# Performance work log

Hardware: AMD Instinct MI355X
Metric: run time of the kernel (lower is better)

The kernel has to match this reference:

```python
import jax, jax.numpy as jnp
import numpy as np

N_NODES = 100000
N_EDGES = 1600000
D_IN = 128
D_EMB = 128


def setup_inputs() -> dict:
    key = jax.random.key(0)
    ks = jax.random.split(key, 8)
    x = jax.random.normal(ks[0], (N_NODES, D_IN), dtype=jnp.float32)
    src = jax.random.randint(ks[1], (N_EDGES,), 0, N_NODES, dtype=jnp.int32)
    dst = jax.random.randint(ks[2], (N_EDGES,), 0, N_NODES, dtype=jnp.int32)
    # Glorot-ish init for GraphConv weights
    s = 1.0 / np.sqrt(D_EMB)
    W0 = jax.random.normal(ks[3], (D_IN, D_EMB), dtype=jnp.float32) * s
    W1 = jax.random.normal(ks[4], (D_EMB, D_EMB), dtype=jnp.float32) * s
    W2 = jax.random.normal(ks[5], (D_EMB, D_EMB), dtype=jnp.float32) * s
    b0 = jnp.zeros((D_EMB,), jnp.float32)
    b1 = jnp.zeros((D_EMB,), jnp.float32)
    b2 = jnp.zeros((D_EMB,), jnp.float32)
    return {"x": x, "src": src, "dst": dst,
            "W0": W0, "b0": b0, "W1": W1, "b1": b1, "W2": W2, "b2": b2}


def _graph_conv(h, src, dst, norm_src, norm_dst, W, b):
    # DGL GraphConv, norm='both': D_out^{-1/2} A D_in^{-1/2} H W + b
    h = h * norm_src[:, None]                       # scale src features
    m = jax.ops.segment_sum(h[src], dst, num_segments=N_NODES)  # SpMM aggregate
    m = m * norm_dst[:, None]
    return m @ W + b


def reference(x, src, dst, W0, b0, W1, b1, W2, b2):
    ones = jnp.ones((N_EDGES,), jnp.float32)
    out_deg = jax.ops.segment_sum(ones, src, num_segments=N_NODES)
    in_deg = jax.ops.segment_sum(ones, dst, num_segments=N_NODES)
    norm_src = jax.lax.rsqrt(jnp.clip(out_deg, 1.0))
    norm_dst = jax.lax.rsqrt(jnp.clip(in_deg, 1.0))

    h = x
    Ws = (W0, W1, W2)
    bs = (b0, b1, b2)
    n_layers = len(Ws)
    for layer in range(n_layers):
        h = _graph_conv(h, src, dst, norm_src, norm_dst, Ws[layer], bs[layer])
        if layer != n_layers - 1:
            h = jax.nn.relu(h)  # dropout is identity in eval mode
    return h
```

## Files before the change

kernel.cpp:

```cpp
#include <hip/hip_runtime.h>
#include <hip/hip_bf16.h>

#define N_NODES 100000
#define N_EDGES 1600000
#define D 128
#define NB 1563
#define PB 512
#define CHUNK 3125
#define SCANL (NB * PB)
#define SGRID (SCANL / 512)
#define SENT N_NODES
#define ECAP_PAD (N_EDGES + 256 * NB)
#define BCAP 2816

typedef __attribute__((ext_vector_type(8))) short bf16x8;
typedef __attribute__((ext_vector_type(4))) float f32x4;

__device__ __forceinline__ float bf2f(unsigned short u) {
    unsigned int x = ((unsigned int)u) << 16;
    return __builtin_bit_cast(float, x);
}
__device__ __forceinline__ unsigned short f2bf(float f) {
    unsigned int x = __builtin_bit_cast(unsigned int, f);
    x += 0x7fffu + ((x >> 16) & 1u);
    return (unsigned short)(x >> 16);
}
__device__ __forceinline__ void accum8(float* acc, uint4 x) {
    acc[0] += bf2f((unsigned short)x.x); acc[1] += bf2f((unsigned short)(x.x >> 16));
    acc[2] += bf2f((unsigned short)x.y); acc[3] += bf2f((unsigned short)(x.y >> 16));
    acc[4] += bf2f((unsigned short)x.z); acc[5] += bf2f((unsigned short)(x.z >> 16));
    acc[6] += bf2f((unsigned short)x.w); acc[7] += bf2f((unsigned short)(x.w >> 16));
}
__device__ __forceinline__ int XP(int b) { return ((b & 7) << 6) | (b >> 3); }

__global__ __launch_bounds__(1024) void k_pcount(const int* __restrict__ src, const int* __restrict__ dst,
                                                 int* __restrict__ cntD, int* __restrict__ cntS) {
    __shared__ int hd[NB];
    __shared__ int hs[NB];
    int t = threadIdx.x, blk = blockIdx.x;
    int col = XP(blk);
    for (int i = t; i < NB; i += 1024) { hd[i] = 0; hs[i] = 0; }
    __syncthreads();
    int base = blk * CHUNK;
    for (int i = t; i < CHUNK; i += 1024) {
        int e = base + i;
        atomicAdd(&hd[dst[e] >> 6], 1);
        atomicAdd(&hs[src[e] >> 6], 1);
    }
    __syncthreads();
    for (int i = t; i < NB; i += 1024) {
        cntD[i * PB + col] = hd[i];
        cntS[i * PB + col] = hs[i];
    }
}

__global__ void k_scanDS1(int* __restrict__ cntD, int* __restrict__ cntS, int* __restrict__ bs) {
    __shared__ int tmp[256];
    int t = threadIdx.x;
    int which = (blockIdx.x >= SGRID) ? 1 : 0;
    int blk = blockIdx.x - which * SGRID;
    int* a = which ? cntS : cntD;
    int base = blk * 512;
    int a0 = a[base + 2 * t], a1 = a[base + 2 * t + 1];
    int s = a0 + a1;
    tmp[t] = s; __syncthreads();
    for (int off = 1; off < 256; off <<= 1) {
        int x = (t >= off) ? tmp[t - off] : 0;
        __syncthreads();
        tmp[t] += x;
        __syncthreads();
    }
    int excl = tmp[t] - s;
    a[base + 2 * t] = excl;
    a[base + 2 * t + 1] = excl + a0;
    if (t == 255) bs[blockIdx.x] = tmp[255];
}

__global__ void k_scan2two(int* __restrict__ bs) {
    __shared__ int tmp[1024];
    int t = threadIdx.x;
    int base = blockIdx.x * SGRID;
    int i0 = 2 * t, i1 = 2 * t + 1;
    int a = (i0 < SGRID) ? bs[base + i0] : 0;
    int b = (i1 < SGRID) ? bs[base + i1] : 0;
    int s = a + b;
    tmp[t] = s; __syncthreads();
    for (int off = 1; off < 1024; off <<= 1) {
        int x = (t >= off) ? tmp[t - off] : 0;
        __syncthreads();
        tmp[t] += x;
        __syncthreads();
    }
    int excl = tmp[t] - s;
    if (i0 < SGRID) bs[base + i0] = excl;
    if (i1 < SGRID) bs[base + i1] = excl + a;
}


__global__ __launch_bounds__(1024) void k_pscatter(const int* __restrict__ src, const int* __restrict__ dst,
                                                   const int* __restrict__ scanD, const int* __restrict__ scanS,
                                                   const int* __restrict__ bs,
                                                   unsigned int* __restrict__ pairD, unsigned char* __restrict__ srcS) {
    __shared__ int od[NB];
    __shared__ int osx[NB];
    int t = threadIdx.x, blk = blockIdx.x;
    int col = XP(blk);
    for (int i = t; i < NB; i += 1024) {
        od[i] = scanD[i * PB + col] + bs[i];
        osx[i] = scanS[i * PB + col] + bs[SGRID + i];
    }
    __syncthreads();
    int base = blk * CHUNK;
    for (int i = t; i < CHUNK; i += 1024) {
        int e = base + i;
        int s = src[e], d = dst[e];
        int pd = atomicAdd(&od[d >> 6], 1);
        pairD[pd] = ((unsigned int)(d & 63) << 26) | (unsigned int)s;
        int ps = atomicAdd(&osx[s >> 6], 1);
        srcS[ps] = (unsigned char)(s & 63);
    }
}

__global__ __launch_bounds__(256) void k_prep(
        const unsigned int* __restrict__ pairD, const unsigned char* __restrict__ srcS,
        const int* __restrict__ scanD, const int* __restrict__ scanS, const int* __restrict__ bs,
        const float* __restrict__ x,
        const float* __restrict__ W0, const float* __restrict__ W1, const float* __restrict__ W2,
        int* __restrict__ esrc, int* __restrict__ rowbeg, int* __restrict__ degD,
        float* __restrict__ norm_src, unsigned short* __restrict__ Wt,
        unsigned short* __restrict__ hA, unsigned short* __restrict__ hB) {
    __shared__ int c[64];
    __shared__ float nsl[64];
    __shared__ int cnt[64], off[64], cur[64];
    __shared__ int ptotS;
    __shared__ int stage[BCAP];
    int b = blockIdx.x, t = threadIdx.x;
    int lane = t & 63, wave = t >> 6;

    if (b < 24) {
        int gid = b * 256 + t;
        int layer = gid >> 11;
        int di8   = gid & 2047;
        const float* W = (layer == 0) ? W0 : ((layer == 1) ? W1 : W2);
        int di   = di8 * 8;
        int wl   = di8 & 63;
        int nt   = (di8 >> 6) & 7;
        int kc   = di8 >> 9;
        int quad = wl >> 4, wcol = wl & 15;
        unsigned short v[8];
#pragma unroll
        for (int j = 0; j < 8; j++) {
            int k = kc * 32 + quad * 8 + j;
            v[j] = f2bf(W[k * 128 + nt * 16 + wcol]);
        }
        unsigned short* dp = Wt + (size_t)layer * 16384 + di;
#pragma unroll
        for (int j = 0; j < 8; j++) dp[j] = v[j];
    }
    if (b == 0 && t < 32) {
        uint4 z = {0u, 0u, 0u, 0u};
        if (t < 16) ((uint4*)(hA + (size_t)SENT * D))[t] = z;
        else        ((uint4*)(hB + (size_t)SENT * D))[t - 16] = z;
    }

    if (t < 64) c[t] = 0;
    __syncthreads();
    int begS = scanS[b * PB] + bs[SGRID + b];
    int endS = (b < NB - 1) ? (scanS[(b + 1) * PB] + bs[SGRID + b + 1]) : N_EDGES;
    for (int i = begS + t; i < endS; i += 256) atomicAdd(&c[srcS[i]], 1);
    __syncthreads();
    if (t < 64) {
        int g = b * 64 + t;
        float nv = 1.f;
        if (g < N_NODES) {
            int a = c[t]; if (a < 1) a = 1;
            nv = rsqrtf((float)a);
            norm_src[g] = nv;
        }
        nsl[t] = nv;
    }
    __syncthreads();

    for (int i = t; i < 2048; i += 256) {
        int row = b * 64 + (i >> 5);
        if (row < N_NODES) {
            float sc = nsl[i >> 5];
            const float4 v = ((const float4*)x)[(size_t)row * 32 + (i & 31)];
            unsigned int lo = (unsigned int)f2bf(v.x * sc) | ((unsigned int)f2bf(v.y * sc) << 16);
            unsigned int hi = (unsigned int)f2bf(v.z * sc) | ((unsigned int)f2bf(v.w * sc) << 16);
            ((uint2*)hA)[(size_t)row * 32 + (i & 31)] = make_uint2(lo, hi);
        }
    }

    if (t < 64) cnt[t] = 0;
    __syncthreads();
    int beg = scanD[b * PB] + bs[b];
    int end = (b < NB - 1) ? (scanD[(b + 1) * PB] + bs[b + 1]) : N_EDGES;
    int n = end - beg;
    int base = beg + 256 * b;
    for (int i = t; i < n; i += 256) atomicAdd(&cnt[pairD[beg + i] >> 26], 1);
    __syncthreads();
    if (wave == 0) {
        int v = cnt[lane];
        int pc = (v + 3) & ~3;
        int xx = pc;
        for (int o = 1; o < 64; o <<= 1) { int y = __shfl_up(xx, o); if (lane >= o) xx += y; }
        off[lane] = xx - pc;
        cur[lane] = xx - pc;
        if (lane == 63) ptotS = xx;
    }
    __syncthreads();
    int ptot = ptotS; if (ptot > BCAP) ptot = BCAP;
    if (t < 64) {
        int g = b * 64 + t;
        if (g < N_NODES) { rowbeg[g] = base + off[t]; degD[g] = cnt[t]; }
    }
    for (int i = t; i < ptot; i += 256) stage[i] = SENT;
    __syncthreads();
    for (int i = t; i < n; i += 256) {
        unsigned int p = pairD[beg + i];
        int pos = atomicAdd(&cur[p >> 26], 1);
        if (pos < BCAP) stage[pos] = (int)(p & 0x3FFFFFFu);
    }
    __syncthreads();
    for (int i = t; i < ptot; i += 256) esrc[base + i] = stage[i];
}

__device__ __forceinline__ int aswz(int row, int byte16) {
    return row * 256 + (byte16 ^ ((row & 7) << 4));
}

__global__ __launch_bounds__(256, 8) void k_fused(const unsigned short* __restrict__ hin,
        const int* __restrict__ esrc, const int* __restrict__ rowbeg, const int* __restrict__ degD,
        const float* __restrict__ nsp,
        const unsigned short* __restrict__ Wt, const float* __restrict__ bias,
        unsigned short* __restrict__ Cb, float* __restrict__ Cf, int M) {
    __shared__ int rb[64];
    __shared__ int dgt[64];
    __shared__ unsigned short lA[64 * 128];
    int b = blockIdx.x, t = threadIdx.x;
    int lane = t & 63, wave = t >> 6;
    int sub = lane >> 4, col = lane & 15;

    if (t < 64) {
        int g = b * 64 + t;
        rb[t]  = (g < M) ? rowbeg[g] : 0;
        dgt[t] = (g < M) ? degD[g] : 0;
    }
    __syncthreads();

    int r = wave;
    int ro = rb[r], dgr = dgt[r];
    int re = ro + ((dgr + 3) & ~3);
    int idxreg = (ro + lane < re) ? esrc[ro + lane] : 0;
    for (int k = 0; k < 16; k++, r += 4) {
        int nro = 0, ndgr = 0, nre = 0, nidx = 0;
        if (k < 15) {
            nro = rb[r + 4]; ndgr = dgt[r + 4];
            nre = nro + ((ndgr + 3) & ~3);
            nidx = (nro + lane < nre) ? esrc[nro + lane] : 0;
        }
        float acc[8];
#pragma unroll
        for (int j = 0; j < 8; j++) acc[j] = 0.f;
        int w = ro;
        int wend = (w + 64 < re) ? (w + 64) : re;
        int e = w;
        while (true) {
            for (; e + 16 <= wend; e += 16) {
                int q = e - w;
                int s0 = __shfl(idxreg, q + sub);
                int s1 = __shfl(idxreg, q + 4 + sub);
                int s2 = __shfl(idxreg, q + 8 + sub);
                int s3 = __shfl(idxreg, q + 12 + sub);
                uint4 x0 = *(const uint4*)(hin + (size_t)s0 * D + col * 8);
                uint4 x1 = *(const uint4*)(hin + (size_t)s1 * D + col * 8);
                uint4 x2 = *(const uint4*)(hin + (size_t)s2 * D + col * 8);
                uint4 x3 = *(const uint4*)(hin + (size_t)s3 * D + col * 8);
                accum8(acc, x0); accum8(acc, x1); accum8(acc, x2); accum8(acc, x3);
            }
            for (; e < wend; e += 4) {
                int q = e - w;
                int s = __shfl(idxreg, q + sub);
                uint4 x = *(const uint4*)(hin + (size_t)s * D + col * 8);
                accum8(acc, x);
            }
            if (wend >= re) break;
            w = wend;
            idxreg = (w + lane < re) ? esrc[w + lane] : 0;
            wend = (w + 64 < re) ? (w + 64) : re;
        }
#pragma unroll
        for (int j = 0; j < 8; j++) {
            acc[j] += __shfl_xor(acc[j], 16);
            acc[j] += __shfl_xor(acc[j], 32);
        }
        if (sub == 0) {
            int d2 = dgr; if (d2 < 1) d2 = 1;
            float s = rsqrtf((float)d2);
            uint4 o;
            o.x = (unsigned int)f2bf(acc[0] * s) | ((unsigned int)f2bf(acc[1] * s) << 16);
            o.y = (unsigned int)f2bf(acc[2] * s) | ((unsigned int)f2bf(acc[3] * s) << 16);
            o.z = (unsigned int)f2bf(acc[4] * s) | ((unsigned int)f2bf(acc[5] * s) << 16);
            o.w = (unsigned int)f2bf(acc[6] * s) | ((unsigned int)f2bf(acc[7] * s) << 16);
            *(uint4*)((char*)lA + aswz(r, col * 16)) = o;
        }
        ro = nro; dgr = ndgr; re = nre; idxreg = nidx;
    }
    __syncthreads();

    int row0 = b * 64 + wave * 16;
    float nsv[4];
    if (Cb) {
#pragma unroll
        for (int rr4 = 0; rr4 < 4; rr4++) {
            int rr = row0 + sub * 4 + rr4;
            nsv[rr4] = (rr < M) ? nsp[rr] : 1.f;
        }
    }
#pragma unroll
    for (int half = 0; half < 2; half++) {
        f32x4 acc2[4];
#pragma unroll
        for (int i = 0; i < 4; i++) acc2[i] = (f32x4){0.f, 0.f, 0.f, 0.f};
        int lr = wave * 16 + col;
#pragma unroll
        for (int kc = 0; kc < 4; kc++) {
            bf16x8 af = *(const bf16x8*)((const char*)lA + aswz(lr, kc * 64 + sub * 16));
#pragma unroll
            for (int j = 0; j < 4; j++) {
                int nt = half * 4 + j;
                bf16x8 bfr = *(const bf16x8*)(Wt + ((size_t)(kc * 8 + nt) * 64 + lane) * 8);
                acc2[j] = __builtin_amdgcn_mfma_f32_16x16x32_bf16(af, bfr, acc2[j], 0, 0, 0);
            }
        }
#pragma unroll
        for (int j = 0; j < 4; j++) {
            int nt = half * 4 + j;
            float bv = bias[nt * 16 + col];
#pragma unroll
            for (int rr4 = 0; rr4 < 4; rr4++) {
                int rr = row0 + sub * 4 + rr4;
                if (rr < M) {
                    float v = acc2[j][rr4] + bv;
                    if (Cf) {
                        Cf[(size_t)rr * D + nt * 16 + col] = v;
                    } else {
                        v = fmaxf(v, 0.f) * nsv[rr4];
                        Cb[(size_t)rr * D + nt * 16 + col] = f2bf(v);
                    }
                }
            }
        }
    }
}

extern "C" void kernel_launch(void* const* d_in, const int* in_sizes, int n_in,
                              void* d_out, int out_size, void* d_ws, size_t ws_size,
                              hipStream_t stream) {
    const float* x  = (const float*)d_in[0];
    const int* src = (const int*)d_in[1];
    const int* dst = (const int*)d_in[2];
    const float* Wl[3] = {(const float*)d_in[3], (const float*)d_in[5], (const float*)d_in[7]};
    const float* Bl[3] = {(const float*)d_in[4], (const float*)d_in[6], (const float*)d_in[8]};

    const int N = N_NODES;
    const int Mpad = ((N + 63) / 64) * 64;
    const size_t HBYTES = (size_t)Mpad * D * 2;

    char* ws = (char*)d_ws;

    unsigned short* hB = (unsigned short*)ws;
    int* cntD = (int*)ws;
    int* cntS = (int*)(ws + (size_t)SCANL * 4);
    unsigned int*  pairD = (unsigned int*)(ws + (size_t)2 * SCANL * 4);
    unsigned char* srcS  = (unsigned char*)(ws + (size_t)2 * SCANL * 4 + (size_t)N_EDGES * 4);
    int* bs = (int*)(ws + (size_t)2 * SCANL * 4 + (size_t)N_EDGES * 5);

    size_t o = HBYTES;
    auto take = [&](size_t bytes) -> void* {
        o = (o + 255) & ~(size_t)255;
        void* p = ws + o;
        o += bytes;
        return p;
    };
    float* norm_src = (float*)take((size_t)N * 4);
    int*   esrc     = (int*)take((size_t)(ECAP_PAD + 256) * 4);
    int*   rowbeg   = (int*)take((size_t)N * 4);
    int*   degD     = (int*)take((size_t)N * 4);
    unsigned short* Wt = (unsigned short*)take((size_t)3 * 128 * 128 * 2);
    unsigned short* hA = (unsigned short*)take(HBYTES);

    k_pcount<<<PB, 1024, 0, stream>>>(src, dst, cntD, cntS);
    k_scanDS1<<<2 * SGRID, 256, 0, stream>>>(cntD, cntS, bs);
    k_scan2two<<<2, 1024, 0, stream>>>(bs);
    k_pscatter<<<PB, 1024, 0, stream>>>(src, dst, cntD, cntS, bs, pairD, srcS);
    k_prep<<<NB, 256, 0, stream>>>(pairD, srcS, cntD, cntS, bs, x,
                                   Wl[0], Wl[1], Wl[2],
                                   esrc, rowbeg, degD, norm_src, Wt, hA, hB);

    k_fused<<<NB, 256, 0, stream>>>(hA, esrc, rowbeg, degD, norm_src, Wt,         Bl[0], hB, nullptr, N);
    k_fused<<<NB, 256, 0, stream>>>(hB, esrc, rowbeg, degD, norm_src, Wt + 16384, Bl[1], hA, nullptr, N);
    k_fused<<<NB, 256, 0, stream>>>(hA, esrc, rowbeg, degD, norm_src, Wt + 32768, Bl[2], nullptr, (float*)d_out, N);
}
```

Baseline: 370.5 us.

## Shrink partition count to 128 and drop row-index prefetch in aggregation loop

Cuts the edge-partitioning grid from 512 to 128 blocks, each handling a larger chunk (12500 edges). This shrinks the count/scan matrices and makes the scan bookkeeping (block sums shared across four buckets, bounds checks) cheaper. It also removes the software prefetch of the next row's edge indices in the SpMM aggregation loop, replacing it with a simpler per-row loop. Fewer partition blocks may underuse the GPU in the count and scatter phases, and dropping the prefetch may expose index-load latency.

```diff
diff --git a/kernel.cpp b/kernel.cpp
--- a/kernel.cpp
+++ b/kernel.cpp
@@ -5,10 +5,10 @@
 #define N_EDGES 1600000
 #define D 128
 #define NB 1563
-#define PB 512
-#define CHUNK 3125
+#define PB 128
+#define CHUNK 12500
 #define SCANL (NB * PB)
-#define SGRID (SCANL / 512)
+#define SGRID 391
 #define SENT N_NODES
 #define ECAP_PAD (N_EDGES + 256 * NB)
 #define BCAP 2816
@@ -31,7 +31,7 @@
     acc[4] += bf2f((unsigned short)x.z); acc[5] += bf2f((unsigned short)(x.z >> 16));
     acc[6] += bf2f((unsigned short)x.w); acc[7] += bf2f((unsigned short)(x.w >> 16));
 }
-__device__ __forceinline__ int XP(int b) { return ((b & 7) << 6) | (b >> 3); }
+__device__ __forceinline__ int XP(int b) { return ((b & 7) << 4) | (b >> 3); }
 
 __global__ __launch_bounds__(1024) void k_pcount(const int* __restrict__ src, const int* __restrict__ dst,
                                                  int* __restrict__ cntD, int* __restrict__ cntS) {
@@ -60,8 +60,9 @@
     int which = (blockIdx.x >= SGRID) ? 1 : 0;
     int blk = blockIdx.x - which * SGRID;
     int* a = which ? cntS : cntD;
-    int base = blk * 512;
-    int a0 = a[base + 2 * t], a1 = a[base + 2 * t + 1];
+    int g0 = blk * 512 + 2 * t, g1 = g0 + 1;
+    int a0 = (g0 < SCANL) ? a[g0] : 0;
+    int a1 = (g1 < SCANL) ? a[g1] : 0;
     int s = a0 + a1;
     tmp[t] = s; __syncthreads();
     for (int off = 1; off < 256; off <<= 1) {
@@ -71,8 +72,8 @@
         __syncthreads();
     }
     int excl = tmp[t] - s;
-    a[base + 2 * t] = excl;
-    a[base + 2 * t + 1] = excl + a0;
+    if (g0 < SCANL) a[g0] = excl;
+    if (g1 < SCANL) a[g1] = excl + a0;
     if (t == 255) bs[blockIdx.x] = tmp[255];
 }
 
@@ -106,8 +107,8 @@
     int t = threadIdx.x, blk = blockIdx.x;
     int col = XP(blk);
     for (int i = t; i < NB; i += 1024) {
-        od[i] = scanD[i * PB + col] + bs[i];
-        osx[i] = scanS[i * PB + col] + bs[SGRID + i];
+        od[i] = scanD[i * PB + col] + bs[i >> 2];
+        osx[i] = scanS[i * PB + col] + bs[SGRID + (i >> 2)];
     }
     __syncthreads();
     int base = blk * CHUNK;
@@ -165,8 +166,8 @@
 
     if (t < 64) c[t] = 0;
     __syncthreads();
-    int begS = scanS[b * PB] + bs[SGRID + b];
-    int endS = (b < NB - 1) ? (scanS[(b + 1) * PB] + bs[SGRID + b + 1]) : N_EDGES;
+    int begS = scanS[b * PB] + bs[SGRID + (b >> 2)];
+    int endS = (b < NB - 1) ? (scanS[(b + 1) * PB] + bs[SGRID + ((b + 1) >> 2)]) : N_EDGES;
     for (int i = begS + t; i < endS; i += 256) atomicAdd(&c[srcS[i]], 1);
     __syncthreads();
     if (t < 64) {
@@ -194,8 +195,8 @@
 
     if (t < 64) cnt[t] = 0;
     __syncthreads();
-    int beg = scanD[b * PB] + bs[b];
-    int end = (b < NB - 1) ? (scanD[(b + 1) * PB] + bs[b + 1]) : N_EDGES;
+    int beg = scanD[b * PB] + bs[b >> 2];
+    int end = (b < NB - 1) ? (scanD[(b + 1) * PB] + bs[(b + 1) >> 2]) : N_EDGES;
     int n = end - beg;
     int base = beg + 256 * b;
     for (int i = t; i < n; i += 256) atomicAdd(&cnt[pairD[beg + i] >> 26], 1);
@@ -249,24 +250,19 @@
     }
     __syncthreads();
 
-    int r = wave;
-    int ro = rb[r], dgr = dgt[r];
-    int re = ro + ((dgr + 3) & ~3);
-    int idxreg = (ro + lane < re) ? esrc[ro + lane] : 0;
-    for (int k = 0; k < 16; k++, r += 4) {
-        int nro = 0, ndgr = 0, nre = 0, nidx = 0;
-        if (k < 15) {
-            nro = rb[r + 4]; ndgr = dgt[r + 4];
-            nre = nro + ((ndgr + 3) & ~3);
-            nidx = (nro + lane < nre) ? esrc[nro + lane] : 0;
-        }
+    for (int r = wave; r < 64; r += 4) {
+        int ro = rb[r];
+        int dgr = dgt[r];
+        int re = ro + ((dgr + 3) & ~3);
         float acc[8];
 #pragma unroll
         for (int j = 0; j < 8; j++) acc[j] = 0.f;
-        int w = ro;
-        int wend = (w + 64 < re) ? (w + 64) : re;
-        int e = w;
-        while (true) {
+        int e = ro;
+        while (e < re) {
+            int w = e;
+            int wl = w + lane;
+            int idxreg = (wl < re) ? esrc[wl] : 0;
+            int wend = (w + 64 < re) ? (w + 64) : re;
             for (; e + 16 <= wend; e += 16) {
                 int q = e - w;
                 int s0 = __shfl(idxreg, q + sub);
@@ -285,10 +281,6 @@
                 uint4 x = *(const uint4*)(hin + (size_t)s * D + col * 8);
                 accum8(acc, x);
             }
-            if (wend >= re) break;
-            w = wend;
-            idxreg = (w + lane < re) ? esrc[w + lane] : 0;
-            wend = (w + 64 < re) ? (w + 64) : re;
         }
 #pragma unroll
         for (int j = 0; j < 8; j++) {
@@ -305,7 +297,6 @@
             o.w = (unsigned int)f2bf(acc[6] * s) | ((unsigned int)f2bf(acc[7] * s) << 16);
             *(uint4*)((char*)lA + aswz(r, col * 16)) = o;
         }
-        ro = nro; dgr = ndgr; re = nre; idxreg = nidx;
     }
     __syncthreads();
 
@@ -313,9 +304,9 @@
     float nsv[4];
     if (Cb) {
 #pragma unroll
-        for (int rr4 = 0; rr4 < 4; rr4++) {
-            int rr = row0 + sub * 4 + rr4;
-            nsv[rr4] = (rr < M) ? nsp[rr] : 1.f;
+        for (int r = 0; r < 4; r++) {
+            int rr = row0 + sub * 4 + r;
+            nsv[r] = (rr < M) ? nsp[rr] : 1.f;
         }
     }
 #pragma unroll
@@ -339,14 +330,14 @@
             int nt = half * 4 + j;
             float bv = bias[nt * 16 + col];
 #pragma unroll
-            for (int rr4 = 0; rr4 < 4; rr4++) {
-                int rr = row0 + sub * 4 + rr4;
+            for (int r = 0; r < 4; r++) {
+                int rr = row0 + sub * 4 + r;
                 if (rr < M) {
-                    float v = acc2[j][rr4] + bv;
+                    float v = acc2[j][r] + bv;
                     if (Cf) {
                         Cf[(size_t)rr * D + nt * 16 + col] = v;
                     } else {
-                        v = fmaxf(v, 0.f) * nsv[rr4];
+                        v = fmaxf(v, 0.f) * nsv[r];
                         Cb[(size_t)rr * D + nt * 16 + col] = f2bf(v);
                     }
                 }
```

Result: no change. 368.7 us (-0.5%).
